# Performance work log

Hardware: AMD Instinct MI355X
Metric: run time of the kernel (lower is better)

Reference implementation:

```python
import jax, jax.numpy as jnp
import numpy as np

N_ATTR = 100000   # rows of ndata (node attribute table)
MAX_Z = 100000    # config['max_z']
ATTR_DIM = 64
HID = 32          # hidden_units
NUM_LAYERS = 3
K = 30            # SortPooling k
B = 1024          # number of graphs in the batch
NPG = 256         # nodes per graph
N = B * NPG       # 262144 total nodes
EPG = 4096        # edges per graph
E = B * EPG       # 4194304 total edges
D_LAT = HID * NUM_LAYERS + 1  # 97
DENSE_DIM = (((K - 2) // 2 + 1) - 5 + 1) * 32  # 352


def setup_inputs() -> dict:
    key = jax.random.key(0)
    ks = jax.random.split(key, 24)
    # edges confined within each subgraph (batched graph structure)
    offs = jnp.repeat(jnp.arange(B, dtype=jnp.int32) * NPG, EPG)
    src = offs + jax.random.randint(ks[0], (E,), 0, NPG, dtype=jnp.int32)
    dst = offs + jax.random.randint(ks[1], (E,), 0, NPG, dtype=jnp.int32)
    node_id = jax.random.randint(ks[2], (N,), 0, min(N_ATTR, MAX_Z))
    feats = jax.random.randint(ks[3], (N,), 0, 1000)  # structural z-labels
    edge_id = jax.random.randint(ks[4], (E,), 0, E)
    ndata = jax.random.normal(ks[5], (N_ATTR, ATTR_DIM), jnp.float32)
    edata = jax.random.uniform(ks[6], (E, 1), jnp.float32)
    node_emb = jax.random.normal(ks[7], (N_ATTR + MAX_Z, HID), jnp.float32) * 0.1
    s = 0.05
    d_in = ATTR_DIM + 2 * HID  # 128
    W0 = jax.random.normal(ks[8], (d_in, HID), jnp.float32) * s
    W1 = jax.random.normal(ks[9], (HID, HID), jnp.float32) * s
    W2 = jax.random.normal(ks[10], (HID, HID), jnp.float32) * s
    W3 = jax.random.normal(ks[11], (HID, 1), jnp.float32) * s
    b0 = jnp.zeros((HID,), jnp.float32)
    b1 = jnp.zeros((HID,), jnp.float32)
    b2 = jnp.zeros((HID,), jnp.float32)
    b3 = jnp.zeros((1,), jnp.float32)
    conv1_w = jax.random.normal(ks[12], (16, 1, D_LAT), jnp.float32) * s
    conv1_b = jnp.zeros((16,), jnp.float32)
    conv2_w = jax.random.normal(ks[13], (32, 16, 5), jnp.float32) * s
    conv2_b = jnp.zeros((32,), jnp.float32)
    fc1_w = jax.random.normal(ks[14], (128, DENSE_DIM), jnp.float32) * s
    fc1_b = jnp.zeros((128,), jnp.float32)
    fc2_w = jax.random.normal(ks[15], (1, 128), jnp.float32) * s
    fc2_b = jnp.zeros((1,), jnp.float32)
    return dict(feats=feats, node_id=node_id, edge_id=edge_id, src=src, dst=dst,
                ndata=ndata, edata=edata, node_emb=node_emb,
                W0=W0, b0=b0, W1=W1, b1=b1, W2=W2, b2=b2, W3=W3, b3=b3,
                conv1_w=conv1_w, conv1_b=conv1_b, conv2_w=conv2_w, conv2_b=conv2_b,
                fc1_w=fc1_w, fc1_b=fc1_b, fc2_w=fc2_w, fc2_b=fc2_b)


def _dgcnn_forward(feats, node_id, edge_id, src, dst, ndata, edata, node_emb,
                   W0, b0, W1, b1, W2, b2, W3, b3,
                   conv1_w, conv1_b, conv2_w, conv2_b, fc1_w, fc1_b, fc2_w, fc2_b):
    # --- input features: 3-way embedding concat ---
    x = jnp.concatenate([ndata[node_id], node_emb[feats],
                         node_emb[N_ATTR + node_id]], axis=1)  # [N, 128]
    ew = edata[edge_id][:, 0]  # [E] edge weights
    # DGL GraphConv norm='both': unweighted degree normalization, clamp(min=1)
    ones = jnp.ones((E,), jnp.float32)
    deg_out = jnp.clip(jax.ops.segment_sum(ones, src, num_segments=N), 1.0)
    deg_in = jnp.clip(jax.ops.segment_sum(ones, dst, num_segments=N), 1.0)
    ns = (deg_out ** -0.5)[:, None]  # src norm
    nd = (deg_in ** -0.5)[:, None]   # dst norm

    def gconv(h, W, b):
        # out = D_in^{-1/2} * scatter_add(dst, (D_out^{-1/2} h)[src] * ew) @ W + b
        m = (h * ns)[src] * ew[:, None]                       # [E, d]
        agg = jax.ops.segment_sum(m, dst, num_segments=N)     # [N, d]
        return jnp.tanh((agg * nd) @ W + b)

    h1 = gconv(x, W0, b0)    # [N, 32]
    h2 = gconv(h1, W1, b1)   # [N, 32]
    h3 = gconv(h2, W2, b2)   # [N, 32]
    h4 = gconv(h3, W3, b3)   # [N, 1]
    feat = jnp.concatenate([h1, h2, h3, h4], axis=-1)  # [N, 97]

    # --- SortPooling (DGL): sort each node's features ascending along feature
    # dim, then take top-K nodes per graph sorted descending by last feature ---
    fs = jnp.sort(feat, axis=-1).reshape(B, NPG, D_LAT)
    keys = fs[:, :, -1]                                  # [B, NPG]
    _, idx = jax.lax.top_k(keys, K)                      # [B, K]
    pooled = jnp.take_along_axis(fs, idx[:, :, None], axis=1)  # [B, K, 97]
    z = pooled.reshape(B, 1, K * D_LAT)                  # [B, 1, 2910]

    # --- CNN: Conv1d(1,16,97,stride 97) -> ReLU -> MaxPool(2,2) -> Conv1d(16,32,5) -> ReLU ---
    dn = ('NCH', 'OIH', 'NCH')
    z = jax.lax.conv_general_dilated(z, conv1_w, (D_LAT,), 'VALID', dimension_numbers=dn)
    z = jax.nn.relu(z + conv1_b[None, :, None])          # [B, 16, 30]
    z = jax.lax.reduce_window(z, -jnp.inf, jax.lax.max, (1, 1, 2), (1, 1, 2), 'VALID')  # [B,16,15]
    z = jax.lax.conv_general_dilated(z, conv2_w, (1,), 'VALID', dimension_numbers=dn)
    z = jax.nn.relu(z + conv2_b[None, :, None])          # [B, 32, 11]

    # --- MLP (dropout is identity in eval) ---
    z = z.reshape(B, -1)                                 # [B, 352]
    z = jax.nn.relu(z @ fc1_w.T + fc1_b)
    return z @ fc2_w.T + fc2_b                           # [B, 1]


def reference(feats, node_id, edge_id, src, dst, ndata, edata, node_emb,
              W0, b0, W1, b1, W2, b2, W3, b3,
              conv1_w, conv1_b, conv2_w, conv2_b, fc1_w, fc1_b, fc2_w, fc2_b):
    return _dgcnn_forward(feats, node_id, edge_id, src, dst, ndata, edata, node_emb,
                          W0, b0, W1, b1, W2, b2, W3, b3,
                          conv1_w, conv1_b, conv2_w, conv2_b, fc1_w, fc1_b, fc2_w, fc2_b)
```

## Files before the change

### kernel.cpp

```cpp
#include <hip/hip_runtime.h>
#include <math.h>

#define NPG    256
#define EPG    4096
#define NGRAPH 1024
#define NATTR  100000

__device__ float g_F[(size_t)NGRAPH * NPG * 100];

#define A_Y      0
#define A_E      36864
#define A_ROWS   69696
#define A_NS     70752
#define A_ND     71776
#define A_BS     72800
#define A_KEYS   73312
#define A_Y4     74336
#define A_SEL    75360
#define A_ORD    75488
#define A_TOTAL  76000

#define E_EWRAW  0
#define E_RAWSD  16384
#define E_DEGI   32768
#define E_DEGO   33792
#define E_CUR    34816

#define H_S30    0
#define H_C1W    12000
#define H_C2W    18208
#define H_L1     28448
#define H_Q      30368
#define H_RR     31328
#define H_FF     32736

__device__ __forceinline__ void aggregate32(const uint2* sE, const int* rowS,
                                            const ushort* ord, const float* Y,
                                            const float* nd, const float* Bs, int boff,
                                            float* keys, float* __restrict__ gFg, int t)
{
    #pragma unroll
    for (int r = 0; r < 2; ++r) {
        const int n = ord[r * 128 + (t >> 3)];
        const int q = t & 7;
        const int rs = rowS[n], re = rowS[n + 1];
        double a0 = 0.0, a1 = 0.0, a2 = 0.0, a3 = 0.0;
        uint2 e0 = sE[rs];
        uint2 e1 = sE[rs + 1];
        float4 y0 = *(const float4*)(Y + e0.y * 36 + q * 4);
        for (int e = rs; e < re; ++e) {
            const float4 y1 = *(const float4*)(Y + e1.y * 36 + q * 4);
            const uint2 e2 = sE[e + 2];
            const double w = (double)__uint_as_float(e0.x);
            a0 += (double)y0.x * w;
            a1 += (double)y0.y * w;
            a2 += (double)y0.z * w;
            a3 += (double)y0.w * w;
            e0 = e1; e1 = e2; y0 = y1;
        }
        const double sc = (double)nd[n];
        float4 hv;
        hv.x = tanhf((float)(a0 * sc) + Bs[boff + q * 4 + 0]);
        hv.y = tanhf((float)(a1 * sc) + Bs[boff + q * 4 + 1]);
        hv.z = tanhf((float)(a2 * sc) + Bs[boff + q * 4 + 2]);
        hv.w = tanhf((float)(a3 * sc) + Bs[boff + q * 4 + 3]);
        *(float4*)(gFg + (size_t)n * 100 + boff + q * 4) = hv;
        float m = fmaxf(fmaxf(hv.x, hv.y), fmaxf(hv.z, hv.w));
        m = fmaxf(m, __shfl_xor(m, 1, 64));
        m = fmaxf(m, __shfl_xor(m, 2, 64));
        m = fmaxf(m, __shfl_xor(m, 4, 64));
        if (q == 0) keys[n] = fmaxf(keys[n], m);
    }
}

extern "C" __global__ void __launch_bounds__(1024, 8)
dgcnn_fused(const int* __restrict__ feats, const int* __restrict__ node_id,
            const int* __restrict__ edge_id, const int* __restrict__ src,
            const int* __restrict__ dst,
            const float* __restrict__ ndata, const float* __restrict__ edata,
            const float* __restrict__ node_emb,
            const float* __restrict__ W0, const float* __restrict__ b0,
            const float* __restrict__ W1, const float* __restrict__ b1,
            const float* __restrict__ W2, const float* __restrict__ b2,
            const float* __restrict__ W3, const float* __restrict__ b3,
            const float* __restrict__ c1w, const float* __restrict__ c1b,
            const float* __restrict__ c2w, const float* __restrict__ c2b,
            const float* __restrict__ f1w, const float* __restrict__ f1b,
            const float* __restrict__ f2w, const float* __restrict__ f2b,
            float* __restrict__ out)
{
    extern __shared__ char smem[];
    float*  Y    = (float*)(smem + A_Y);
    uint2*  sE   = (uint2*)(smem + A_E);
    int*    rowS = (int*)(smem + A_ROWS);
    float*  ns   = (float*)(smem + A_NS);
    float*  nd   = (float*)(smem + A_ND);
    float*  Bs   = (float*)(smem + A_BS);
    float*  keys = (float*)(smem + A_KEYS);
    float*  y4   = (float*)(smem + A_Y4);
    int*    selI = (int*)(smem + A_SEL);
    ushort* ord  = (ushort*)(smem + A_ORD);

    const int g = blockIdx.x, t = threadIdx.x;
    const int lane = t & 63, wv = t >> 6;
    float* gFg = g_F + (size_t)g * NPG * 100;

    float* ewRaw = (float*)((char*)Y + E_EWRAW);
    uint*  rawSD = (uint*)((char*)Y + E_RAWSD);
    int*   degI  = (int*)((char*)Y + E_DEGI);
    int*   degO  = (int*)((char*)Y + E_DEGO);
    int*   cur   = (int*)((char*)Y + E_CUR);

    if (t < NPG) { degI[t] = 0; degO[t] = 0; keys[t] = -INFINITY; }
    if (t < 97) Bs[t] = (t < 32) ? b0[t] : (t < 64) ? b1[t - 32]
                       : (t < 96) ? b2[t - 64] : b3[0];
    if (t < 4) sE[4096 + t] = make_uint2(0u, 0u);
    __syncthreads();
    for (int e = t; e < EPG; e += 1024) {
        const int ge = g * EPG + e;
        const int s = src[ge] - g * NPG;
        const int d = dst[ge] - g * NPG;
        rawSD[e] = (uint)s | ((uint)d << 16);
        ewRaw[e] = edata[edge_id[ge]];
        atomicAdd(&degO[s], 1);
        atomicAdd(&degI[d], 1);
    }
    __syncthreads();
    if (t < 64) {
        const int d0 = degI[4 * t], d1 = degI[4 * t + 1],
                  d2 = degI[4 * t + 2], d3 = degI[4 * t + 3];
        const int p1 = d0, p2 = p1 + d1, p3 = p2 + d2, p4 = p3 + d3;
        int s = p4;
        #pragma unroll
        for (int off = 1; off <= 32; off <<= 1) {
            const int o = __shfl_up(s, off, 64);
            if (lane >= off) s += o;
        }
        const int excl = s - p4;
        rowS[4 * t + 1] = excl + p1;
        rowS[4 * t + 2] = excl + p2;
        rowS[4 * t + 3] = excl + p3;
        rowS[4 * t + 4] = excl + p4;
        if (t == 0) rowS[0] = 0;
    }
    __syncthreads();
    if (t < NPG) {
        ns[t] = (float)(1.0 / sqrt((double)(degO[t] > 0 ? degO[t] : 1)));
        nd[t] = (float)(1.0 / sqrt((double)(degI[t] > 0 ? degI[t] : 1)));
        cur[t] = rowS[t];
    }
    __syncthreads();
    for (int e = t; e < EPG; e += 1024) {
        const uint sd = rawSD[e];
        const int d = (int)(sd >> 16), s = (int)(sd & 0xffffu);
        const int pos = atomicAdd(&cur[d], 1);
        sE[pos] = make_uint2(__float_as_uint(ewRaw[e]), (uint)s);
    }
    __syncthreads();
    if (t < NPG) degO[t] = 0;
    __syncthreads();
    if (t < NPG) atomicAdd(&degO[min(degI[t], 255)], 1);
    __syncthreads();
    if (t < 64) {
        const int d0 = degO[4 * t], d1 = degO[4 * t + 1],
                  d2 = degO[4 * t + 2], d3 = degO[4 * t + 3];
        const int p1 = d0, p2 = p1 + d1, p3 = p2 + d2, p4 = p3 + d3;
        int s = p4;
        #pragma unroll
        for (int off = 1; off <= 32; off <<= 1) {
            const int o = __shfl_up(s, off, 64);
            if (lane >= off) s += o;
        }
        const int excl = s - p4;
        cur[4 * t]     = excl;
        cur[4 * t + 1] = excl + p1;
        cur[4 * t + 2] = excl + p2;
        cur[4 * t + 3] = excl + p3;
    }
    __syncthreads();
    if (t < NPG) {
        const int pos = atomicAdd(&cur[min(degI[t], 255)], 1);
        ord[pos] = (ushort)t;
    }
    __syncthreads();

    const int j = t & 31, nb = t >> 5;

    {
        float acc[8] = {0.f, 0.f, 0.f, 0.f, 0.f, 0.f, 0.f, 0.f};
        for (int c = 0; c < 4; ++c) {
            for (int i = t; i < 2048; i += 1024) {
                const int n = i >> 3, q = i & 7;
                const int gn = g * NPG + n;
                const int nidn = node_id[gn];
                const int j0 = c * 32 + q * 4;
                float4 v;
                if (j0 < 64)      v = *(const float4*)(ndata    + (size_t)nidn * 64 + j0);
                else if (j0 < 96) v = *(const float4*)(node_emb + (size_t)feats[gn] * 32 + (j0 - 64));
                else              v = *(const float4*)(node_emb + (size_t)(NATTR + nidn) * 32 + (j0 - 96));
                const float sc = ns[n];
                float4 o; o.x = v.x * sc; o.y = v.y * sc; o.z = v.z * sc; o.w = v.w * sc;
                *(float4*)(Y + n * 36 + q * 4) = o;
            }
            __syncthreads();
            float wc[32];
            #pragma unroll
            for (int d = 0; d < 32; ++d) wc[d] = W0[(c * 32 + d) * 32 + j];
            #pragma unroll
            for (int i2 = 0; i2 < 8; ++i2) {
                const int n = nb * 8 + i2;
                const float4* ar = (const float4*)(Y + n * 36);
                float a = acc[i2];
                #pragma unroll
                for (int d8 = 0; d8 < 8; ++d8) {
                    const float4 av = ar[d8];
                    a = fmaf(av.x, wc[4 * d8 + 0], a);
                    a = fmaf(av.y, wc[4 * d8 + 1], a);
                    a = fmaf(av.z, wc[4 * d8 + 2], a);
                    a = fmaf(av.w, wc[4 * d8 + 3], a);
                }
                acc[i2] = a;
            }
            __syncthreads();
        }
        #pragma unroll
        for (int i2 = 0; i2 < 8; ++i2) Y[(nb * 8 + i2) * 36 + j] = acc[i2];
        __syncthreads();
        aggregate32(sE, rowS, ord, Y, nd, Bs, 0, keys, gFg, t);
        __syncthreads();
    }

    for (int L = 0; L < 2; ++L) {
        const float* WL = L ? W2 : W1;
        const int pb = L ? 32 : 0;
        float wc[32];
        #pragma unroll
        for (int d = 0; d < 32; ++d) wc[d] = WL[d * 32 + j];
        float acc[8];
        #pragma unroll
        for (int i2 = 0; i2 < 8; ++i2) {
            const int n = nb * 8 + i2;
            const float4* fr = (const float4*)(gFg + (size_t)n * 100 + pb);
            float a = 0.f;
            #pragma unroll
            for (int d8 = 0; d8 < 8; ++d8) {
                const float4 av = fr[d8];
                a = fmaf(av.x, wc[4 * d8 + 0], a);
                a = fmaf(av.y, wc[4 * d8 + 1], a);
                a = fmaf(av.z, wc[4 * d8 + 2], a);
                a = fmaf(av.w, wc[4 * d8 + 3], a);
            }
            acc[i2] = a * ns[n];
        }
        __syncthreads();
        #pragma unroll
        for (int i2 = 0; i2 < 8; ++i2) Y[(nb * 8 + i2) * 36 + j] = acc[i2];
        __syncthreads();
        aggregate32(sE, rowS, ord, Y, nd, Bs, 32 + L * 32, keys, gFg, t);
        __syncthreads();
    }

    if (t < NPG) {
        const float4* fr = (const float4*)(gFg + (size_t)t * 100 + 64);
        float a = 0.f;
        #pragma unroll
        for (int d8 = 0; d8 < 8; ++d8) {
            const float4 h = fr[d8];
            a = fmaf(h.x, W3[4 * d8 + 0], a);
            a = fmaf(h.y, W3[4 * d8 + 1], a);
            a = fmaf(h.z, W3[4 * d8 + 2], a);
            a = fmaf(h.w, W3[4 * d8 + 3], a);
        }
        y4[t] = a * ns[t];
    }
    __syncthreads();
    {
        const int n = ord[t >> 2], p = t & 3;
        const int rs = rowS[n], re = rowS[n + 1];
        double a = 0.0;
        for (int e = rs + p; e < re; e += 4) {
            const uint2 ed = sE[e];
            a += (double)__uint_as_float(ed.x) * (double)y4[ed.y];
        }
        a += __shfl_xor(a, 1, 64);
        a += __shfl_xor(a, 2, 64);
        if (p == 0) {
            const float h = tanhf((float)(a * (double)nd[n]) + Bs[96]);
            gFg[(size_t)n * 100 + 96] = h;
            keys[n] = fmaxf(keys[n], h);
        }
    }
    __syncthreads();

    char*  HB   = (char*)Y;
    float* S30  = (float*)(HB + H_S30);
    float* c1wS = (float*)(HB + H_C1W);
    float* c2wS = (float*)(HB + H_C2W);
    float* L1   = (float*)(HB + H_L1);
    float* Q    = (float*)(HB + H_Q);
    float* Rr   = (float*)(HB + H_RR);
    float* Ff   = (float*)(HB + H_FF);

    if (t < 64) {
        float kv[4]; int ki[4];
        #pragma unroll
        for (int r = 0; r < 4; ++r) { ki[r] = lane * 4 + r; kv[r] = keys[lane * 4 + r]; }
        for (int it = 0; it < 30; ++it) {
            float bv = kv[0]; int bi = ki[0];
            #pragma unroll
            for (int r = 1; r < 4; ++r)
                if (kv[r] > bv || (kv[r] == bv && ki[r] < bi)) { bv = kv[r]; bi = ki[r]; }
            #pragma unroll
            for (int off = 1; off <= 32; off <<= 1) {
                const float ov = __shfl_xor(bv, off, 64);
                const int   oi = __shfl_xor(bi, off, 64);
                if (ov > bv || (ov == bv && oi < bi)) { bv = ov; bi = oi; }
            }
            if (lane == 0) selI[it] = bi;
            if ((bi >> 2) == lane) kv[bi & 3] = -INFINITY;
        }
    } else {
        for (int i = t - 64; i < 1552; i += 960) c1wS[i] = c1w[i];
        for (int i = t - 64; i < 2560; i += 960) c2wS[i] = c2w[i];
    }
    __syncthreads();

    for (int k = wv; k < 30; k += 16) {
        const float* fr = gFg + (size_t)selI[k] * 100;
        float v0 = fr[lane];
        float v1 = (lane < 33) ? fr[64 + lane] : INFINITY;
        for (int kk = 2; kk <= 128; kk <<= 1) {
            for (int jj = kk >> 1; jj > 0; jj >>= 1) {
                if (jj == 64) {
                    const float lo = fminf(v0, v1), hi = fmaxf(v0, v1);
                    v0 = lo; v1 = hi;
                } else {
                    const float p0 = __shfl_xor(v0, jj, 64);
                    const float p1 = __shfl_xor(v1, jj, 64);
                    const bool up   = ((lane & jj) == 0);
                    const bool asc0 = (kk == 128) ? true : ((lane & kk) == 0);
                    const bool asc1 = (kk == 128) ? true : (((64 + lane) & kk) == 0);
                    v0 = (up == asc0) ? fminf(v0, p0) : fmaxf(v0, p0);
                    v1 = (up == asc1) ? fminf(v1, p1) : fmaxf(v1, p1);
                }
            }
        }
        S30[k * 100 + lane] = v0;
        if (lane < 33) S30[k * 100 + 64 + lane] = v1;
    }
    __syncthreads();

    if (t < 480) {
        const int k = t >> 4, c = t & 15;
        const float* row  = S30 + k * 100;
        const float* wrow = c1wS + c * 97;
        float acc = c1b[c];
        for (int d = 0; d < 97; ++d) acc = fmaf(row[d], wrow[d], acc);
        L1[k * 16 + c] = fmaxf(acc, 0.f);
    }
    __syncthreads();
    if (t < 240) {
        const int c = t / 15, tt = t % 15;
        Q[c * 15 + tt] = fmaxf(L1[(2 * tt) * 16 + c], L1[(2 * tt + 1) * 16 + c]);
    }
    __syncthreads();
    if (t < 352) {
        const int o = t / 11, tt = t % 11;
        const float* wo = c2wS + o * 80;
        float acc = c2b[o];
        #pragma unroll
        for (int c = 0; c < 16; ++c)
            #pragma unroll
            for (int jj = 0; jj < 5; ++jj)
                acc = fmaf(Q[c * 15 + tt + jj], wo[c * 5 + jj], acc);
        Rr[o * 11 + tt] = fmaxf(acc, 0.f);
    }
    __syncthreads();
    if (t < 128) {
        float acc = f1b[t];
        const float* wr = f1w + t * 352;
        for (int i = 0; i < 352; ++i) acc = fmaf(Rr[i], wr[i], acc);
        Ff[t] = fmaxf(acc, 0.f);
    }
    __syncthreads();
    if (t < 64) {
        float acc = Ff[lane] * f2w[lane] + Ff[lane + 64] * f2w[lane + 64];
        #pragma unroll
        for (int off = 1; off <= 32; off <<= 1) acc += __shfl_xor(acc, off, 64);
        if (lane == 0) out[g] = acc + f2b[0];
    }
}

extern "C" void kernel_launch(void* const* d_in, const int* in_sizes, int n_in,
                              void* d_out, int out_size, void* d_ws, size_t ws_size,
                              hipStream_t stream)
{
    const int*   feats    = (const int*)d_in[0];
    const int*   node_id  = (const int*)d_in[1];
    const int*   edge_id  = (const int*)d_in[2];
    const int*   src      = (const int*)d_in[3];
    const int*   dst      = (const int*)d_in[4];
    const float* ndata    = (const float*)d_in[5];
    const float* edata    = (const float*)d_in[6];
    const float* node_emb = (const float*)d_in[7];
    const float* W0 = (const float*)d_in[8];
    const float* b0 = (const float*)d_in[9];
    const float* W1 = (const float*)d_in[10];
    const float* b1 = (const float*)d_in[11];
    const float* W2 = (const float*)d_in[12];
    const float* b2 = (const float*)d_in[13];
    const float* W3 = (const float*)d_in[14];
    const float* b3 = (const float*)d_in[15];
    const float* c1w = (const float*)d_in[16];
    const float* c1b = (const float*)d_in[17];
    const float* c2w = (const float*)d_in[18];
    const float* c2b = (const float*)d_in[19];
    const float* f1w = (const float*)d_in[20];
    const float* f1b = (const float*)d_in[21];
    const float* f2w = (const float*)d_in[22];
    const float* f2b = (const float*)d_in[23];

    (void)hipFuncSetAttribute((const void*)dgcnn_fused,
                              hipFuncAttributeMaxDynamicSharedMemorySize, A_TOTAL);

    dgcnn_fused<<<NGRAPH, 1024, A_TOTAL, stream>>>(feats, node_id, edge_id, src, dst,
                                                   ndata, edata, node_emb,
                                                   W0, b0, W1, b1, W2, b2, W3, b3,
                                                   c1w, c1b, c2w, c2b,
                                                   f1w, f1b, f2w, f2b,
                                                   (float*)d_out);
}
```

Baseline: 370.0 us.

## Split fused DGCNN kernel into edge-prep, GNN-layer, and head kernels

The single fused per-graph kernel becomes three launches. Edge preparation (CSR build, degree norms, degree ordering) and the SortPooling/conv/MLP head move into separate 512-thread kernels that pass data through global scratch buffers. The aim is to let each phase run at its own occupancy and block size, instead of idling most of a 1024-thread block during serial phases. The cost is extra global-memory round trips for the edge list, row offsets and keys, plus the overhead of two more launches.

```diff
diff --git a/kernel.cpp b/kernel.cpp
--- a/kernel.cpp
+++ b/kernel.cpp
@@ -6,7 +6,97 @@
 #define NGRAPH 1024
 #define NATTR  100000
 
-__device__ float g_F[(size_t)NGRAPH * NPG * 100];
+__device__ float  g_F[(size_t)NGRAPH * NPG * 100];
+__device__ uint2  g_E[(size_t)NGRAPH * 4104];
+__device__ int    g_rows[(size_t)NGRAPH * 257];
+__device__ float  g_ns[(size_t)NGRAPH * NPG];
+__device__ float  g_nd[(size_t)NGRAPH * NPG];
+__device__ ushort g_ord[(size_t)NGRAPH * NPG];
+__device__ float  g_keys[(size_t)NGRAPH * NPG];
+
+extern "C" __global__ void __launch_bounds__(512, 8)
+edge_prep(const int* __restrict__ src, const int* __restrict__ dst,
+          const int* __restrict__ edge_id, const float* __restrict__ edata)
+{
+    __shared__ float ewRaw[4096];
+    __shared__ uint  rawSD[4096];
+    __shared__ int   degI[256], degO[256], cur[256], rowSs[257];
+
+    const int g = blockIdx.x, t = threadIdx.x;
+    const int lane = t & 63;
+    uint2* gEg = g_E + (size_t)g * 4104;
+
+    if (t < NPG) { degI[t] = 0; degO[t] = 0; }
+    __syncthreads();
+    for (int e = t; e < EPG; e += 512) {
+        const int ge = g * EPG + e;
+        const int s = src[ge] - g * NPG;
+        const int d = dst[ge] - g * NPG;
+        rawSD[e] = (uint)s | ((uint)d << 16);
+        ewRaw[e] = edata[edge_id[ge]];
+        atomicAdd(&degO[s], 1);
+        atomicAdd(&degI[d], 1);
+    }
+    __syncthreads();
+    if (t < 64) {
+        const int d0 = degI[4 * t], d1 = degI[4 * t + 1],
+                  d2 = degI[4 * t + 2], d3 = degI[4 * t + 3];
+        const int p1 = d0, p2 = p1 + d1, p3 = p2 + d2, p4 = p3 + d3;
+        int s = p4;
+        #pragma unroll
+        for (int off = 1; off <= 32; off <<= 1) {
+            const int o = __shfl_up(s, off, 64);
+            if (lane >= off) s += o;
+        }
+        const int excl = s - p4;
+        rowSs[4 * t + 1] = excl + p1;
+        rowSs[4 * t + 2] = excl + p2;
+        rowSs[4 * t + 3] = excl + p3;
+        rowSs[4 * t + 4] = excl + p4;
+        if (t == 0) rowSs[0] = 0;
+    }
+    __syncthreads();
+    if (t < NPG) {
+        g_ns[g * NPG + t] = (float)(1.0 / sqrt((double)(degO[t] > 0 ? degO[t] : 1)));
+        g_nd[g * NPG + t] = (float)(1.0 / sqrt((double)(degI[t] > 0 ? degI[t] : 1)));
+        cur[t] = rowSs[t];
+    }
+    if (t < 257) g_rows[g * 257 + t] = rowSs[t];
+    if (t < 8)   gEg[4096 + t] = make_uint2(0u, 0u);
+    __syncthreads();
+    for (int e = t; e < EPG; e += 512) {
+        const uint sd = rawSD[e];
+        const int d = (int)(sd >> 16), s = (int)(sd & 0xffffu);
+        const int pos = atomicAdd(&cur[d], 1);
+        gEg[pos] = make_uint2(__float_as_uint(ewRaw[e]), (uint)s);
+    }
+    __syncthreads();
+    if (t < NPG) degO[t] = 0;
+    __syncthreads();
+    if (t < NPG) atomicAdd(&degO[min(degI[t], 255)], 1);
+    __syncthreads();
+    if (t < 64) {
+        const int d0 = degO[4 * t], d1 = degO[4 * t + 1],
+                  d2 = degO[4 * t + 2], d3 = degO[4 * t + 3];
+        const int p1 = d0, p2 = p1 + d1, p3 = p2 + d2, p4 = p3 + d3;
+        int s = p4;
+        #pragma unroll
+        for (int off = 1; off <= 32; off <<= 1) {
+            const int o = __shfl_up(s, off, 64);
+            if (lane >= off) s += o;
+        }
+        const int excl = s - p4;
+        cur[4 * t]     = excl;
+        cur[4 * t + 1] = excl + p1;
+        cur[4 * t + 2] = excl + p2;
+        cur[4 * t + 3] = excl + p3;
+    }
+    __syncthreads();
+    if (t < NPG) {
+        const int pos = atomicAdd(&cur[min(degI[t], 255)], 1);
+        g_ord[g * NPG + pos] = (ushort)t;
+    }
+}
 
 #define A_Y      0
 #define A_E      36864
@@ -16,23 +106,8 @@
 #define A_BS     72800
 #define A_KEYS   73312
 #define A_Y4     74336
-#define A_SEL    75360
-#define A_ORD    75488
-#define A_TOTAL  76000
-
-#define E_EWRAW  0
-#define E_RAWSD  16384
-#define E_DEGI   32768
-#define E_DEGO   33792
-#define E_CUR    34816
-
-#define H_S30    0
-#define H_C1W    12000
-#define H_C2W    18208
-#define H_L1     28448
-#define H_Q      30368
-#define H_RR     31328
-#define H_FF     32736
+#define A_ORD    75360
+#define A_TOTAL  75904
 
 __device__ __forceinline__ void aggregate32(const uint2* sE, const int* rowS,
                                             const ushort* ord, const float* Y,
@@ -74,20 +149,12 @@
 }
 
 extern "C" __global__ void __launch_bounds__(1024, 8)
-dgcnn_fused(const int* __restrict__ feats, const int* __restrict__ node_id,
-            const int* __restrict__ edge_id, const int* __restrict__ src,
-            const int* __restrict__ dst,
-            const float* __restrict__ ndata, const float* __restrict__ edata,
-            const float* __restrict__ node_emb,
-            const float* __restrict__ W0, const float* __restrict__ b0,
-            const float* __restrict__ W1, const float* __restrict__ b1,
-            const float* __restrict__ W2, const float* __restrict__ b2,
-            const float* __restrict__ W3, const float* __restrict__ b3,
-            const float* __restrict__ c1w, const float* __restrict__ c1b,
-            const float* __restrict__ c2w, const float* __restrict__ c2b,
-            const float* __restrict__ f1w, const float* __restrict__ f1b,
-            const float* __restrict__ f2w, const float* __restrict__ f2b,
-            float* __restrict__ out)
+gnn_layers(const int* __restrict__ feats, const int* __restrict__ node_id,
+           const float* __restrict__ ndata, const float* __restrict__ node_emb,
+           const float* __restrict__ W0, const float* __restrict__ b0,
+           const float* __restrict__ W1, const float* __restrict__ b1,
+           const float* __restrict__ W2, const float* __restrict__ b2,
+           const float* __restrict__ W3, const float* __restrict__ b3)
 {
     extern __shared__ char smem[];
     float*  Y    = (float*)(smem + A_Y);
@@ -98,90 +165,22 @@
     float*  Bs   = (float*)(smem + A_BS);
     float*  keys = (float*)(smem + A_KEYS);
     float*  y4   = (float*)(smem + A_Y4);
-    int*    selI = (int*)(smem + A_SEL);
     ushort* ord  = (ushort*)(smem + A_ORD);
 
     const int g = blockIdx.x, t = threadIdx.x;
-    const int lane = t & 63, wv = t >> 6;
     float* gFg = g_F + (size_t)g * NPG * 100;
-
-    float* ewRaw = (float*)((char*)Y + E_EWRAW);
-    uint*  rawSD = (uint*)((char*)Y + E_RAWSD);
-    int*   degI  = (int*)((char*)Y + E_DEGI);
-    int*   degO  = (int*)((char*)Y + E_DEGO);
-    int*   cur   = (int*)((char*)Y + E_CUR);
-
-    if (t < NPG) { degI[t] = 0; degO[t] = 0; keys[t] = -INFINITY; }
+    const uint2* gEg = g_E + (size_t)g * 4104;
+
+    for (int i = t; i < 4104; i += 1024) sE[i] = gEg[i];
+    if (t < 257) rowS[t] = g_rows[g * 257 + t];
+    if (t < NPG) {
+        ns[t] = g_ns[g * NPG + t];
+        nd[t] = g_nd[g * NPG + t];
+        ord[t] = g_ord[g * NPG + t];
+        keys[t] = -INFINITY;
+    }
     if (t < 97) Bs[t] = (t < 32) ? b0[t] : (t < 64) ? b1[t - 32]
                        : (t < 96) ? b2[t - 64] : b3[0];
-    if (t < 4) sE[4096 + t] = make_uint2(0u, 0u);
-    __syncthreads();
-    for (int e = t; e < EPG; e += 1024) {
-        const int ge = g * EPG + e;
-        const int s = src[ge] - g * NPG;
-        const int d = dst[ge] - g * NPG;
-        rawSD[e] = (uint)s | ((uint)d << 16);
-        ewRaw[e] = edata[edge_id[ge]];
-        atomicAdd(&degO[s], 1);
-        atomicAdd(&degI[d], 1);
-    }
-    __syncthreads();
-    if (t < 64) {
-        const int d0 = degI[4 * t], d1 = degI[4 * t + 1],
-                  d2 = degI[4 * t + 2], d3 = degI[4 * t + 3];
-        const int p1 = d0, p2 = p1 + d1, p3 = p2 + d2, p4 = p3 + d3;
-        int s = p4;
-        #pragma unroll
-        for (int off = 1; off <= 32; off <<= 1) {
-            const int o = __shfl_up(s, off, 64);
-            if (lane >= off) s += o;
-        }
-        const int excl = s - p4;
-        rowS[4 * t + 1] = excl + p1;
-        rowS[4 * t + 2] = excl + p2;
-        rowS[4 * t + 3] = excl + p3;
-        rowS[4 * t + 4] = excl + p4;
-        if (t == 0) rowS[0] = 0;
-    }
-    __syncthreads();
-    if (t < NPG) {
-        ns[t] = (float)(1.0 / sqrt((double)(degO[t] > 0 ? degO[t] : 1)));
-        nd[t] = (float)(1.0 / sqrt((double)(degI[t] > 0 ? degI[t] : 1)));
-        cur[t] = rowS[t];
-    }
-    __syncthreads();
-    for (int e = t; e < EPG; e += 1024) {
-        const uint sd = rawSD[e];
-        const int d = (int)(sd >> 16), s = (int)(sd & 0xffffu);
-        const int pos = atomicAdd(&cur[d], 1);
-        sE[pos] = make_uint2(__float_as_uint(ewRaw[e]), (uint)s);
-    }
-    __syncthreads();
-    if (t < NPG) degO[t] = 0;
-    __syncthreads();
-    if (t < NPG) atomicAdd(&degO[min(degI[t], 255)], 1);
-    __syncthreads();
-    if (t < 64) {
-        const int d0 = degO[4 * t], d1 = degO[4 * t + 1],
-                  d2 = degO[4 * t + 2], d3 = degO[4 * t + 3];
-        const int p1 = d0, p2 = p1 + d1, p3 = p2 + d2, p4 = p3 + d3;
-        int s = p4;
-        #pragma unroll
-        for (int off = 1; off <= 32; off <<= 1) {
-            const int o = __shfl_up(s, off, 64);
-            if (lane >= off) s += o;
-        }
-        const int excl = s - p4;
-        cur[4 * t]     = excl;
-        cur[4 * t + 1] = excl + p1;
-        cur[4 * t + 2] = excl + p2;
-        cur[4 * t + 3] = excl + p3;
-    }
-    __syncthreads();
-    if (t < NPG) {
-        const int pos = atomicAdd(&cur[min(degI[t], 255)], 1);
-        ord[pos] = (ushort)t;
-    }
     __syncthreads();
 
     const int j = t & 31, nb = t >> 5;
@@ -291,15 +290,32 @@
         }
     }
     __syncthreads();
-
-    char*  HB   = (char*)Y;
-    float* S30  = (float*)(HB + H_S30);
-    float* c1wS = (float*)(HB + H_C1W);
-    float* c2wS = (float*)(HB + H_C2W);
-    float* L1   = (float*)(HB + H_L1);
-    float* Q    = (float*)(HB + H_Q);
-    float* Rr   = (float*)(HB + H_RR);
-    float* Ff   = (float*)(HB + H_FF);
+    if (t < NPG) g_keys[g * NPG + t] = keys[t];
+}
+
+extern "C" __global__ void __launch_bounds__(512, 8)
+head_kernel(const float* __restrict__ c1w, const float* __restrict__ c1b,
+            const float* __restrict__ c2w, const float* __restrict__ c2b,
+            const float* __restrict__ f1w, const float* __restrict__ f1b,
+            const float* __restrict__ f2w, const float* __restrict__ f2b,
+            float* __restrict__ out)
+{
+    __shared__ float keys[256];
+    __shared__ int   selI[32];
+    __shared__ float S30[30 * 100];
+    __shared__ float c1wS[1552];
+    __shared__ float c2wS[2560];
+    __shared__ float L1[480];
+    __shared__ float Q[240];
+    __shared__ float Rr[352];
+    __shared__ float Ff[128];
+
+    const int g = blockIdx.x, t = threadIdx.x;
+    const int lane = t & 63, wv = t >> 6;
+    const float* gFg = g_F + (size_t)g * NPG * 100;
+
+    if (t < NPG) keys[t] = g_keys[g * NPG + t];
+    __syncthreads();
 
     if (t < 64) {
         float kv[4]; int ki[4];
@@ -320,12 +336,12 @@
             if ((bi >> 2) == lane) kv[bi & 3] = -INFINITY;
         }
     } else {
-        for (int i = t - 64; i < 1552; i += 960) c1wS[i] = c1w[i];
-        for (int i = t - 64; i < 2560; i += 960) c2wS[i] = c2w[i];
-    }
-    __syncthreads();
-
-    for (int k = wv; k < 30; k += 16) {
+        for (int i = t - 64; i < 1552; i += 448) c1wS[i] = c1w[i];
+        for (int i = t - 64; i < 2560; i += 448) c2wS[i] = c2w[i];
+    }
+    __syncthreads();
+
+    for (int k = wv; k < 30; k += 8) {
         const float* fr = gFg + (size_t)selI[k] * 100;
         float v0 = fr[lane];
         float v1 = (lane < 33) ? fr[64 + lane] : INFINITY;
@@ -420,13 +436,13 @@
     const float* f2w = (const float*)d_in[22];
     const float* f2b = (const float*)d_in[23];
 
-    (void)hipFuncSetAttribute((const void*)dgcnn_fused,
+    (void)hipFuncSetAttribute((const void*)gnn_layers,
                               hipFuncAttributeMaxDynamicSharedMemorySize, A_TOTAL);
 
-    dgcnn_fused<<<NGRAPH, 1024, A_TOTAL, stream>>>(feats, node_id, edge_id, src, dst,
-                                                   ndata, edata, node_emb,
-                                                   W0, b0, W1, b1, W2, b2, W3, b3,
-                                                   c1w, c1b, c2w, c2b,
-                                                   f1w, f1b, f2w, f2b,
-                                                   (float*)d_out);
+    edge_prep<<<NGRAPH, 512, 0, stream>>>(src, dst, edge_id, edata);
+    gnn_layers<<<NGRAPH, 1024, A_TOTAL, stream>>>(feats, node_id, ndata, node_emb,
+                                                  W0, b0, W1, b1, W2, b2, W3, b3);
+    head_kernel<<<NGRAPH, 512, 0, stream>>>(c1w, c1b, c2w, c2b,
+                                            f1w, f1b, f2w, f2b,
+                                            (float*)d_out);
 }
```

Result: slower. 386.6 us (+4.5%).

## Keep layer activations in shared memory and balance aggregation across waves

Applied to the files above, without the earlier changes.

Layer outputs are now written back into the shared Y buffer, pre-scaled by the source norm, so the next layer's matvec reads shared memory in place instead of re-reading the global scratch buffer. Each thread now aggregates two nodes chosen from opposite ends of the degree-sorted order (low and high degree), and their indices, row bounds and norms are hoisted out of the layer loop. The input feature gather is register-prefetched one chunk ahead of the matvec. The aggregation loop is unrolled by two without the old cross-iteration prefetch, and the padding entries past the end of the edge list are dropped.

```diff
diff --git a/kernel.cpp b/kernel.cpp
--- a/kernel.cpp
+++ b/kernel.cpp
@@ -10,15 +10,15 @@
 
 #define A_Y      0
 #define A_E      36864
-#define A_ROWS   69696
-#define A_NS     70752
-#define A_ND     71776
-#define A_BS     72800
-#define A_KEYS   73312
-#define A_Y4     74336
-#define A_SEL    75360
-#define A_ORD    75488
-#define A_TOTAL  76000
+#define A_ROWS   69632
+#define A_NS     70688
+#define A_ND     71712
+#define A_BS     72736
+#define A_KEYS   73248
+#define A_Y4     74272
+#define A_SEL    75296
+#define A_ORD    75424
+#define A_TOTAL  75936
 
 #define E_EWRAW  0
 #define E_RAWSD  16384
@@ -34,43 +34,62 @@
 #define H_RR     31328
 #define H_FF     32736
 
-__device__ __forceinline__ void aggregate32(const uint2* sE, const int* rowS,
-                                            const ushort* ord, const float* Y,
-                                            const float* nd, const float* Bs, int boff,
-                                            float* keys, float* __restrict__ gFg, int t)
+__device__ __forceinline__ float4 agg_node(const uint2* sE, int rs, int re,
+                                           const float* Y, int q, float ndn,
+                                           const float* Bs, int boff)
 {
+    double a0 = 0.0, a1 = 0.0, a2 = 0.0, a3 = 0.0;
+    int e = rs;
+    for (; e + 2 <= re; e += 2) {
+        const uint2 ea = sE[e], eb = sE[e + 1];
+        const float4 ya = *(const float4*)(Y + ea.y * 36 + q * 4);
+        const float4 yb = *(const float4*)(Y + eb.y * 36 + q * 4);
+        const double wa = (double)__uint_as_float(ea.x);
+        const double wb = (double)__uint_as_float(eb.x);
+        a0 += (double)ya.x * wa; a1 += (double)ya.y * wa;
+        a2 += (double)ya.z * wa; a3 += (double)ya.w * wa;
+        a0 += (double)yb.x * wb; a1 += (double)yb.y * wb;
+        a2 += (double)yb.z * wb; a3 += (double)yb.w * wb;
+    }
+    if (e < re) {
+        const uint2 ea = sE[e];
+        const float4 ya = *(const float4*)(Y + ea.y * 36 + q * 4);
+        const double wa = (double)__uint_as_float(ea.x);
+        a0 += (double)ya.x * wa; a1 += (double)ya.y * wa;
+        a2 += (double)ya.z * wa; a3 += (double)ya.w * wa;
+    }
+    const double sc = (double)ndn;
+    float4 hv;
+    hv.x = tanhf((float)(a0 * sc) + Bs[boff + q * 4 + 0]);
+    hv.y = tanhf((float)(a1 * sc) + Bs[boff + q * 4 + 1]);
+    hv.z = tanhf((float)(a2 * sc) + Bs[boff + q * 4 + 2]);
+    hv.w = tanhf((float)(a3 * sc) + Bs[boff + q * 4 + 3]);
+    return hv;
+}
+
+__device__ __forceinline__ void matvec_inplace(float* Y, const float* __restrict__ W,
+                                               int j, int nb)
+{
+    float wc[32];
     #pragma unroll
-    for (int r = 0; r < 2; ++r) {
-        const int n = ord[r * 128 + (t >> 3)];
-        const int q = t & 7;
-        const int rs = rowS[n], re = rowS[n + 1];
-        double a0 = 0.0, a1 = 0.0, a2 = 0.0, a3 = 0.0;
-        uint2 e0 = sE[rs];
-        uint2 e1 = sE[rs + 1];
-        float4 y0 = *(const float4*)(Y + e0.y * 36 + q * 4);
-        for (int e = rs; e < re; ++e) {
-            const float4 y1 = *(const float4*)(Y + e1.y * 36 + q * 4);
-            const uint2 e2 = sE[e + 2];
-            const double w = (double)__uint_as_float(e0.x);
-            a0 += (double)y0.x * w;
-            a1 += (double)y0.y * w;
-            a2 += (double)y0.z * w;
-            a3 += (double)y0.w * w;
-            e0 = e1; e1 = e2; y0 = y1;
-        }
-        const double sc = (double)nd[n];
-        float4 hv;
-        hv.x = tanhf((float)(a0 * sc) + Bs[boff + q * 4 + 0]);
-        hv.y = tanhf((float)(a1 * sc) + Bs[boff + q * 4 + 1]);
-        hv.z = tanhf((float)(a2 * sc) + Bs[boff + q * 4 + 2]);
-        hv.w = tanhf((float)(a3 * sc) + Bs[boff + q * 4 + 3]);
-        *(float4*)(gFg + (size_t)n * 100 + boff + q * 4) = hv;
-        float m = fmaxf(fmaxf(hv.x, hv.y), fmaxf(hv.z, hv.w));
-        m = fmaxf(m, __shfl_xor(m, 1, 64));
-        m = fmaxf(m, __shfl_xor(m, 2, 64));
-        m = fmaxf(m, __shfl_xor(m, 4, 64));
-        if (q == 0) keys[n] = fmaxf(keys[n], m);
-    }
+    for (int d = 0; d < 32; ++d) wc[d] = W[d * 32 + j];
+    float acc[8];
+    #pragma unroll
+    for (int i2 = 0; i2 < 8; ++i2) {
+        const float4* ar = (const float4*)(Y + (nb * 8 + i2) * 36);
+        float a = 0.f;
+        #pragma unroll
+        for (int d8 = 0; d8 < 8; ++d8) {
+            const float4 av = ar[d8];
+            a = fmaf(av.x, wc[4 * d8 + 0], a);
+            a = fmaf(av.y, wc[4 * d8 + 1], a);
+            a = fmaf(av.z, wc[4 * d8 + 2], a);
+            a = fmaf(av.w, wc[4 * d8 + 3], a);
+        }
+        acc[i2] = a;
+    }
+    #pragma unroll
+    for (int i2 = 0; i2 < 8; ++i2) Y[(nb * 8 + i2) * 36 + j] = acc[i2];
 }
 
 extern "C" __global__ void __launch_bounds__(1024, 8)
@@ -105,102 +124,127 @@
     const int lane = t & 63, wv = t >> 6;
     float* gFg = g_F + (size_t)g * NPG * 100;
 
-    float* ewRaw = (float*)((char*)Y + E_EWRAW);
-    uint*  rawSD = (uint*)((char*)Y + E_RAWSD);
-    int*   degI  = (int*)((char*)Y + E_DEGI);
-    int*   degO  = (int*)((char*)Y + E_DEGO);
-    int*   cur   = (int*)((char*)Y + E_CUR);
-
-    if (t < NPG) { degI[t] = 0; degO[t] = 0; keys[t] = -INFINITY; }
-    if (t < 97) Bs[t] = (t < 32) ? b0[t] : (t < 64) ? b1[t - 32]
-                       : (t < 96) ? b2[t - 64] : b3[0];
-    if (t < 4) sE[4096 + t] = make_uint2(0u, 0u);
-    __syncthreads();
-    for (int e = t; e < EPG; e += 1024) {
-        const int ge = g * EPG + e;
-        const int s = src[ge] - g * NPG;
-        const int d = dst[ge] - g * NPG;
-        rawSD[e] = (uint)s | ((uint)d << 16);
-        ewRaw[e] = edata[edge_id[ge]];
-        atomicAdd(&degO[s], 1);
-        atomicAdd(&degI[d], 1);
-    }
-    __syncthreads();
-    if (t < 64) {
-        const int d0 = degI[4 * t], d1 = degI[4 * t + 1],
-                  d2 = degI[4 * t + 2], d3 = degI[4 * t + 3];
-        const int p1 = d0, p2 = p1 + d1, p3 = p2 + d2, p4 = p3 + d3;
-        int s = p4;
-        #pragma unroll
-        for (int off = 1; off <= 32; off <<= 1) {
-            const int o = __shfl_up(s, off, 64);
-            if (lane >= off) s += o;
-        }
-        const int excl = s - p4;
-        rowS[4 * t + 1] = excl + p1;
-        rowS[4 * t + 2] = excl + p2;
-        rowS[4 * t + 3] = excl + p3;
-        rowS[4 * t + 4] = excl + p4;
-        if (t == 0) rowS[0] = 0;
-    }
-    __syncthreads();
-    if (t < NPG) {
-        ns[t] = (float)(1.0 / sqrt((double)(degO[t] > 0 ? degO[t] : 1)));
-        nd[t] = (float)(1.0 / sqrt((double)(degI[t] > 0 ? degI[t] : 1)));
-        cur[t] = rowS[t];
-    }
-    __syncthreads();
-    for (int e = t; e < EPG; e += 1024) {
-        const uint sd = rawSD[e];
-        const int d = (int)(sd >> 16), s = (int)(sd & 0xffffu);
-        const int pos = atomicAdd(&cur[d], 1);
-        sE[pos] = make_uint2(__float_as_uint(ewRaw[e]), (uint)s);
-    }
-    __syncthreads();
-    if (t < NPG) degO[t] = 0;
-    __syncthreads();
-    if (t < NPG) atomicAdd(&degO[min(degI[t], 255)], 1);
-    __syncthreads();
-    if (t < 64) {
-        const int d0 = degO[4 * t], d1 = degO[4 * t + 1],
-                  d2 = degO[4 * t + 2], d3 = degO[4 * t + 3];
-        const int p1 = d0, p2 = p1 + d1, p3 = p2 + d2, p4 = p3 + d3;
-        int s = p4;
-        #pragma unroll
-        for (int off = 1; off <= 32; off <<= 1) {
-            const int o = __shfl_up(s, off, 64);
-            if (lane >= off) s += o;
-        }
-        const int excl = s - p4;
-        cur[4 * t]     = excl;
-        cur[4 * t + 1] = excl + p1;
-        cur[4 * t + 2] = excl + p2;
-        cur[4 * t + 3] = excl + p3;
-    }
-    __syncthreads();
-    if (t < NPG) {
-        const int pos = atomicAdd(&cur[min(degI[t], 255)], 1);
-        ord[pos] = (ushort)t;
-    }
-    __syncthreads();
+    {
+        float* ewRaw = (float*)((char*)Y + E_EWRAW);
+        uint*  rawSD = (uint*)((char*)Y + E_RAWSD);
+        int*   degI  = (int*)((char*)Y + E_DEGI);
+        int*   degO  = (int*)((char*)Y + E_DEGO);
+        int*   cur   = (int*)((char*)Y + E_CUR);
+
+        if (t < NPG) { degI[t] = 0; degO[t] = 0; keys[t] = -INFINITY; }
+        if (t < 97) Bs[t] = (t < 32) ? b0[t] : (t < 64) ? b1[t - 32]
+                           : (t < 96) ? b2[t - 64] : b3[0];
+        __syncthreads();
+        for (int e = t; e < EPG; e += 1024) {
+            const int ge = g * EPG + e;
+            const int s = src[ge] - g * NPG;
+            const int d = dst[ge] - g * NPG;
+            rawSD[e] = (uint)s | ((uint)d << 16);
+            ewRaw[e] = edata[edge_id[ge]];
+            atomicAdd(&degO[s], 1);
+            atomicAdd(&degI[d], 1);
+        }
+        __syncthreads();
+        if (t < 64) {
+            const int d0 = degI[4 * t], d1 = degI[4 * t + 1],
+                      d2 = degI[4 * t + 2], d3 = degI[4 * t + 3];
+            const int p1 = d0, p2 = p1 + d1, p3 = p2 + d2, p4 = p3 + d3;
+            int s = p4;
+            #pragma unroll
+            for (int off = 1; off <= 32; off <<= 1) {
+                const int o = __shfl_up(s, off, 64);
+                if (lane >= off) s += o;
+            }
+            const int excl = s - p4;
+            rowS[4 * t + 1] = excl + p1;
+            rowS[4 * t + 2] = excl + p2;
+            rowS[4 * t + 3] = excl + p3;
+            rowS[4 * t + 4] = excl + p4;
+            if (t == 0) rowS[0] = 0;
+        }
+        __syncthreads();
+        if (t < NPG) {
+            ns[t] = (float)(1.0 / sqrt((double)(degO[t] > 0 ? degO[t] : 1)));
+            nd[t] = (float)(1.0 / sqrt((double)(degI[t] > 0 ? degI[t] : 1)));
+            cur[t] = rowS[t];
+        }
+        __syncthreads();
+        for (int e = t; e < EPG; e += 1024) {
+            const uint sd = rawSD[e];
+            const int d = (int)(sd >> 16), s = (int)(sd & 0xffffu);
+            const int pos = atomicAdd(&cur[d], 1);
+            sE[pos] = make_uint2(__float_as_uint(ewRaw[e]), (uint)s);
+        }
+        __syncthreads();
+        if (t < NPG) degO[t] = 0;
+        __syncthreads();
+        if (t < NPG) atomicAdd(&degO[min(degI[t], 255)], 1);
+        __syncthreads();
+        if (t < 64) {
+            const int d0 = degO[4 * t], d1 = degO[4 * t + 1],
+                      d2 = degO[4 * t + 2], d3 = degO[4 * t + 3];
+            const int p1 = d0, p2 = p1 + d1, p3 = p2 + d2, p4 = p3 + d3;
+            int s = p4;
+            #pragma unroll
+            for (int off = 1; off <= 32; off <<= 1) {
+                const int o = __shfl_up(s, off, 64);
+                if (lane >= off) s += o;
+            }
+            const int excl = s - p4;
+            cur[4 * t]     = excl;
+            cur[4 * t + 1] = excl + p1;
+            cur[4 * t + 2] = excl + p2;
+            cur[4 * t + 3] = excl + p3;
+        }
+        __syncthreads();
+        if (t < NPG) {
+            const int pos = atomicAdd(&cur[min(degI[t], 255)], 1);
+            ord[pos] = (ushort)t;
+        }
+        __syncthreads();
+    }
 
     const int j = t & 31, nb = t >> 5;
+    const int q = t & 7, g3 = (t >> 3) & 7;
+    const int n0 = ord[wv * 8 + g3];
+    const int n1 = ord[(31 - wv) * 8 + g3];
+    const int rs0 = rowS[n0], re0 = rowS[n0 + 1];
+    const int rs1 = rowS[n1], re1 = rowS[n1 + 1];
+    const float nd0 = nd[n0], nd1 = nd[n1];
+    const float ns0 = ns[n0], ns1 = ns[n1];
 
     {
+        const int na_ = t >> 3;
+        const int nb2 = na_ + 128;
+        const int gna = g * NPG + na_, gnb = g * NPG + nb2;
+        const int nidA = node_id[gna], fidA = feats[gna];
+        const int nidB = node_id[gnb], fidB = feats[gnb];
+        const float sa = ns[na_], sb = ns[nb2];
+
+        float4 xa, xb;
+        {
+            xa = *(const float4*)(ndata + (size_t)nidA * 64 + q * 4);
+            xb = *(const float4*)(ndata + (size_t)nidB * 64 + q * 4);
+        }
         float acc[8] = {0.f, 0.f, 0.f, 0.f, 0.f, 0.f, 0.f, 0.f};
+        #pragma unroll
         for (int c = 0; c < 4; ++c) {
-            for (int i = t; i < 2048; i += 1024) {
-                const int n = i >> 3, q = i & 7;
-                const int gn = g * NPG + n;
-                const int nidn = node_id[gn];
-                const int j0 = c * 32 + q * 4;
-                float4 v;
-                if (j0 < 64)      v = *(const float4*)(ndata    + (size_t)nidn * 64 + j0);
-                else if (j0 < 96) v = *(const float4*)(node_emb + (size_t)feats[gn] * 32 + (j0 - 64));
-                else              v = *(const float4*)(node_emb + (size_t)(NATTR + nidn) * 32 + (j0 - 96));
-                const float sc = ns[n];
-                float4 o; o.x = v.x * sc; o.y = v.y * sc; o.z = v.z * sc; o.w = v.w * sc;
-                *(float4*)(Y + n * 36 + q * 4) = o;
+            float4 oa; oa.x = xa.x * sa; oa.y = xa.y * sa; oa.z = xa.z * sa; oa.w = xa.w * sa;
+            float4 ob; ob.x = xb.x * sb; ob.y = xb.y * sb; ob.z = xb.z * sb; ob.w = xb.w * sb;
+            *(float4*)(Y + na_ * 36 + q * 4) = oa;
+            *(float4*)(Y + nb2 * 36 + q * 4) = ob;
+            if (c < 3) {
+                const int j0 = (c + 1) * 32 + q * 4;
+                if (j0 < 64) {
+                    xa = *(const float4*)(ndata + (size_t)nidA * 64 + j0);
+                    xb = *(const float4*)(ndata + (size_t)nidB * 64 + j0);
+                } else if (j0 < 96) {
+                    xa = *(const float4*)(node_emb + (size_t)fidA * 32 + (j0 - 64));
+                    xb = *(const float4*)(node_emb + (size_t)fidB * 32 + (j0 - 64));
+                } else {
+                    xa = *(const float4*)(node_emb + (size_t)(NATTR + nidA) * 32 + (j0 - 96));
+                    xb = *(const float4*)(node_emb + (size_t)(NATTR + nidB) * 32 + (j0 - 96));
+                }
             }
             __syncthreads();
             float wc[32];
@@ -208,8 +252,7 @@
             for (int d = 0; d < 32; ++d) wc[d] = W0[(c * 32 + d) * 32 + j];
             #pragma unroll
             for (int i2 = 0; i2 < 8; ++i2) {
-                const int n = nb * 8 + i2;
-                const float4* ar = (const float4*)(Y + n * 36);
+                const float4* ar = (const float4*)(Y + (nb * 8 + i2) * 36);
                 float a = acc[i2];
                 #pragma unroll
                 for (int d8 = 0; d8 < 8; ++d8) {
@@ -226,42 +269,41 @@
         #pragma unroll
         for (int i2 = 0; i2 < 8; ++i2) Y[(nb * 8 + i2) * 36 + j] = acc[i2];
         __syncthreads();
-        aggregate32(sE, rowS, ord, Y, nd, Bs, 0, keys, gFg, t);
-        __syncthreads();
-    }
-
-    for (int L = 0; L < 2; ++L) {
-        const float* WL = L ? W2 : W1;
-        const int pb = L ? 32 : 0;
-        float wc[32];
-        #pragma unroll
-        for (int d = 0; d < 32; ++d) wc[d] = WL[d * 32 + j];
-        float acc[8];
-        #pragma unroll
-        for (int i2 = 0; i2 < 8; ++i2) {
-            const int n = nb * 8 + i2;
-            const float4* fr = (const float4*)(gFg + (size_t)n * 100 + pb);
-            float a = 0.f;
-            #pragma unroll
-            for (int d8 = 0; d8 < 8; ++d8) {
-                const float4 av = fr[d8];
-                a = fmaf(av.x, wc[4 * d8 + 0], a);
-                a = fmaf(av.y, wc[4 * d8 + 1], a);
-                a = fmaf(av.z, wc[4 * d8 + 2], a);
-                a = fmaf(av.w, wc[4 * d8 + 3], a);
-            }
-            acc[i2] = a * ns[n];
-        }
-        __syncthreads();
-        #pragma unroll
-        for (int i2 = 0; i2 < 8; ++i2) Y[(nb * 8 + i2) * 36 + j] = acc[i2];
-        __syncthreads();
-        aggregate32(sE, rowS, ord, Y, nd, Bs, 32 + L * 32, keys, gFg, t);
-        __syncthreads();
+    }
+
+    #pragma unroll 1
+    for (int L = 0; L < 3; ++L) {
+        const int boff = L * 32;
+        const float4 h0 = agg_node(sE, rs0, re0, Y, q, nd0, Bs, boff);
+        const float4 h1 = agg_node(sE, rs1, re1, Y, q, nd1, Bs, boff);
+        *(float4*)(gFg + (size_t)n0 * 100 + boff + q * 4) = h0;
+        *(float4*)(gFg + (size_t)n1 * 100 + boff + q * 4) = h1;
+        float m0 = fmaxf(fmaxf(h0.x, h0.y), fmaxf(h0.z, h0.w));
+        float m1 = fmaxf(fmaxf(h1.x, h1.y), fmaxf(h1.z, h1.w));
+        m0 = fmaxf(m0, __shfl_xor(m0, 1, 64));
+        m0 = fmaxf(m0, __shfl_xor(m0, 2, 64));
+        m0 = fmaxf(m0, __shfl_xor(m0, 4, 64));
+        m1 = fmaxf(m1, __shfl_xor(m1, 1, 64));
+        m1 = fmaxf(m1, __shfl_xor(m1, 2, 64));
+        m1 = fmaxf(m1, __shfl_xor(m1, 4, 64));
+        if (q == 0) {
+            keys[n0] = fmaxf(keys[n0], m0);
+            keys[n1] = fmaxf(keys[n1], m1);
+        }
+        __syncthreads();
+        float4 w0v; w0v.x = h0.x * ns0; w0v.y = h0.y * ns0; w0v.z = h0.z * ns0; w0v.w = h0.w * ns0;
+        float4 w1v; w1v.x = h1.x * ns1; w1v.y = h1.y * ns1; w1v.z = h1.z * ns1; w1v.w = h1.w * ns1;
+        *(float4*)(Y + n0 * 36 + q * 4) = w0v;
+        *(float4*)(Y + n1 * 36 + q * 4) = w1v;
+        __syncthreads();
+        if (L < 2) {
+            matvec_inplace(Y, L ? W2 : W1, j, nb);
+            __syncthreads();
+        }
     }
 
     if (t < NPG) {
-        const float4* fr = (const float4*)(gFg + (size_t)t * 100 + 64);
+        const float4* fr = (const float4*)(Y + t * 36);
         float a = 0.f;
         #pragma unroll
         for (int d8 = 0; d8 < 8; ++d8) {
@@ -271,7 +313,7 @@
             a = fmaf(h.z, W3[4 * d8 + 2], a);
             a = fmaf(h.w, W3[4 * d8 + 3], a);
         }
-        y4[t] = a * ns[t];
+        y4[t] = a;
     }
     __syncthreads();
     {
```

After: 806.8 us. +118.0%, slower.
